# Optimization experiments

Hardware: AMD Instinct MI355X
Metric: run time of the kernel (lower is better)

## Reference

```python
import jax, jax.numpy as jnp
import numpy as np

N_ENT, N_REL, D, H, N_MID = 4096, 200, 128, 4, 9  # 1 input layer + 9 middle layers + 1 out layer
ALPHA = 0.2
NEG = -9e15


def gat_head(x, adj_mask, W, a):
    # x: [N, Fin], W: [Fin, Fout], a: [2*Fout]
    Wh = x @ W                                   # [N, Fout]
    d = Wh.shape[-1]
    f1 = Wh @ a[:d]                              # [N]
    f2 = Wh @ a[d:]                              # [N]
    e = jax.nn.leaky_relu(f1[:, None] + f2[None, :], ALPHA)  # [N, N]
    e = jnp.where(adj_mask, e, NEG)
    attn = jax.nn.softmax(e, axis=-1)
    return attn @ Wh                             # [N, Fout]


def multihead_concat(x, adj_mask, Ws, As):
    # Ws: [H, Fin, Fout], As: [H, 2*Fout] -> elu(concat over heads) [N, H*Fout]
    heads = jax.vmap(lambda W, a: gat_head(x, adj_mask, W, a))(Ws, As)  # [H, N, Fout]
    N = x.shape[0]
    return jax.nn.elu(jnp.transpose(heads, (1, 0, 2)).reshape(N, -1))


def setup_inputs() -> dict:
    key = jax.random.key(0)
    ks = jax.random.split(key, 12)
    s = 0.1
    return {
        "head": jax.random.randint(ks[0], (4096,), 0, N_ENT),
        "relation": jax.random.randint(ks[1], (4096,), 0, N_REL),
        "adj": jax.random.normal(ks[2], (N_ENT, N_ENT), dtype=jnp.float32),
        "entity_emb": jax.random.normal(ks[3], (N_ENT, D), dtype=jnp.float32) * s,
        "relation_emb": jax.random.normal(ks[4], (N_REL, D), dtype=jnp.float32) * s,
        "W0": jax.random.normal(ks[5], (H, D, D), dtype=jnp.float32) * s,
        "a0": jax.random.normal(ks[6], (H, 2 * D), dtype=jnp.float32) * s,
        "Wm": jax.random.normal(ks[7], (N_MID, H, H * D, D), dtype=jnp.float32) * s,
        "am": jax.random.normal(ks[8], (N_MID, H, 2 * D), dtype=jnp.float32) * s,
        "Wo": jax.random.normal(ks[9], (H * D, D), dtype=jnp.float32) * s,
        "ao": jax.random.normal(ks[10], (2 * D,), dtype=jnp.float32) * s,
    }


def reference(head, relation, adj, entity_emb, relation_emb, W0, a0, Wm, am, Wo, ao):
    adj_mask = adj > 0
    # layer 0: D -> H*D
    x = multihead_concat(entity_emb, adj_mask, W0, a0)
    # 9 middle layers: H*D -> H*D (identical shapes -> scan)
    def step(x, params):
        Ws, As = params
        return multihead_concat(x, adj_mask, Ws, As), None
    x, _ = jax.lax.scan(step, x, (Wm, am))
    # output layer: single head H*D -> D, elu applied after
    x = jax.nn.elu(gat_head(x, adj_mask, Wo, ao))
    head_relation_combined = entity_emb[head] + relation_emb[relation]
    return (x, head_relation_combined)
```

## Files before the change

kernel.cpp:

```cpp
#include <hip/hip_runtime.h>

typedef unsigned short u16;
typedef short bf16x8 __attribute__((ext_vector_type(8)));
typedef float f32x4 __attribute__((ext_vector_type(4)));

__device__ __forceinline__ float bf2f(unsigned v) { return __uint_as_float(v << 16); }
__device__ __forceinline__ u16 f2bf(float f) {
    unsigned u = __float_as_uint(f);
    return (u16)((u + 0x7fffu + ((u >> 16) & 1u)) >> 16);
}

__device__ __forceinline__ void gload_lds16(const void* g, void* l) {
    __builtin_amdgcn_global_load_lds(
        (const __attribute__((address_space(1))) unsigned int*)g,
        (__attribute__((address_space(3))) unsigned int*)l, 16, 0, 0);
}

__global__ __launch_bounds__(256) void k_mask(const float* __restrict__ adj,
                                              unsigned* __restrict__ mask) {
    int w = blockIdx.x * 256 + threadIdx.x;
    const float4* q = (const float4*)(adj + (size_t)w * 32);
    unsigned bits = 0u;
#pragma unroll
    for (int i = 0; i < 8; i++) {
        float4 v = q[i];
        if (v.x > 0.f) bits |= (1u << (i * 4 + 0));
        if (v.y > 0.f) bits |= (1u << (i * 4 + 1));
        if (v.z > 0.f) bits |= (1u << (i * 4 + 2));
        if (v.w > 0.f) bits |= (1u << (i * 4 + 3));
    }
    mask[w] = bits;
}

__global__ void k_trans(const float* __restrict__ in, u16* __restrict__ out, int K) {
    __shared__ float t[32][33];
    const float* src = in + (size_t)blockIdx.z * K * 128;
    u16* dst = out + (size_t)blockIdx.z * K * 128;
    int k0 = blockIdx.x * 32, n0 = blockIdx.y * 32;
    int tx = threadIdx.x, ty = threadIdx.y;
#pragma unroll
    for (int i = 0; i < 32; i += 8) t[ty + i][tx] = src[(size_t)(k0 + ty + i) * 128 + n0 + tx];
    __syncthreads();
#pragma unroll
    for (int i = 0; i < 32; i += 8) dst[(size_t)(n0 + ty + i) * K + k0 + tx] = f2bf(t[tx][ty + i]);
}

__global__ __launch_bounds__(256) void k_cvt(const float* __restrict__ in,
                                             u16* __restrict__ out) {
    int t = blockIdx.x * 256 + threadIdx.x;
    float4 v = ((const float4*)in)[t];
    uint2 o;
    o.x = (unsigned)f2bf(v.x) | ((unsigned)f2bf(v.y) << 16);
    o.y = (unsigned)f2bf(v.z) | ((unsigned)f2bf(v.w) << 16);
    ((uint2*)out)[t] = o;
}

__global__ __launch_bounds__(1024, 4) void k_proj(const u16* __restrict__ X,
                                                  const u16* __restrict__ WT,
                                                  const float* __restrict__ avec,
                                                  u16* __restrict__ WhT,
                                                  float* __restrict__ f1,
                                                  float* __restrict__ f2, int Fin) {
    __shared__ u16 As[2][64 * 32];
    __shared__ u16 Bs[2][128 * 32];
    __shared__ float fpart[4][64][2];
    const int tid = threadIdx.x;
    const int wv = tid >> 6, lane = tid & 63;
    const int rg = wv & 3, cg = wv >> 2;
    const int c = lane & 15, quad = lane >> 4;
    const int h = blockIdx.y;
    const int j0 = blockIdx.x * 64;
    const u16* Wp = WT + (size_t)h * 128 * Fin;

#define PROJ_STAGE(buf, kb)                                                              \
    do {                                                                                 \
        if (cg == 0)                                                                     \
            gload_lds16(X + (size_t)(j0 + rg * 16 + (lane >> 2)) * Fin + (kb) + (lane & 3) * 8, \
                        (void*)&As[buf][rg * 16 * 32]);                                  \
        else if (cg <= 2)                                                                \
            gload_lds16(Wp + (size_t)((cg - 1) * 64 + rg * 16 + (lane >> 2)) * Fin + (kb) + (lane & 3) * 8, \
                        (void*)&Bs[buf][((cg - 1) * 64 + rg * 16) * 32]);                \
    } while (0)

    PROJ_STAGE(0, 0);
    __syncthreads();

    f32x4 acc[2];
    acc[0] = (f32x4){0.f, 0.f, 0.f, 0.f};
    acc[1] = (f32x4){0.f, 0.f, 0.f, 0.f};

    int it = 0;
    for (int kb = 0; kb < Fin; kb += 32, it++) {
        const int cur = it & 1;
        if (kb + 32 < Fin) PROJ_STAGE(cur ^ 1, kb + 32);
        bf16x8 av = *(const bf16x8*)&As[cur][(rg * 16 + c) * 32 + quad * 8];
#pragma unroll
        for (int e = 0; e < 2; e++) {
            bf16x8 bv = *(const bf16x8*)&Bs[cur][((cg * 2 + e) * 16 + c) * 32 + quad * 8];
            acc[e] = __builtin_amdgcn_mfma_f32_16x16x32_bf16(av, bv, acc[e], 0, 0, 0);
        }
        __syncthreads();
    }

    u16* Wo = WhT + (size_t)h * 128 * 4096;
    const float* ah = avec + h * 256;
    float p1[4] = {0, 0, 0, 0}, p2[4] = {0, 0, 0, 0};
#pragma unroll
    for (int e = 0; e < 2; e++) {
        const int n = (cg * 2 + e) * 16 + c;
        float a1 = ah[n];
        float a2 = ah[128 + n];
        u16 w4[4];
#pragma unroll
        for (int r = 0; r < 4; r++) {
            float v = acc[e][r];
            w4[r] = f2bf(v);
            p1[r] += v * a1;
            p2[r] += v * a2;
        }
        uint2 pk;
        pk.x = (unsigned)w4[0] | ((unsigned)w4[1] << 16);
        pk.y = (unsigned)w4[2] | ((unsigned)w4[3] << 16);
        *(uint2*)&Wo[(size_t)n * 4096 + j0 + rg * 16 + quad * 4] = pk;
    }
#pragma unroll
    for (int off = 1; off < 16; off <<= 1) {
#pragma unroll
        for (int r = 0; r < 4; r++) {
            p1[r] += __shfl_xor(p1[r], off);
            p2[r] += __shfl_xor(p2[r], off);
        }
    }
    if (c == 0) {
#pragma unroll
        for (int r = 0; r < 4; r++) {
            fpart[cg][rg * 16 + quad * 4 + r][0] = p1[r];
            fpart[cg][rg * 16 + quad * 4 + r][1] = p2[r];
        }
    }
    __syncthreads();
    if (tid < 64) {
        float s1 = fpart[0][tid][0] + fpart[1][tid][0] + fpart[2][tid][0] + fpart[3][tid][0];
        float s2 = fpart[0][tid][1] + fpart[1][tid][1] + fpart[2][tid][1] + fpart[3][tid][1];
        f1[h * 4096 + j0 + tid] = s1;
        f2[h * 4096 + j0 + tid] = s2;
    }
}

template <bool F32OUT>
__global__ __launch_bounds__(1024, 4) void k_attn(const u16* __restrict__ WhT,
                                                  const float* __restrict__ f1g,
                                                  const float* __restrict__ f2g,
                                                  const unsigned char* __restrict__ maskb,
                                                  void* __restrict__ outp, int ostride) {
    __shared__ float f2s[4096];
    __shared__ unsigned char ms[64 * 528];
    __shared__ u16 Bs[2][4][128 * 32];
    __shared__ float f1s[64];
    __shared__ float lpart[4][64];
    __shared__ float redmax[16];
    __shared__ float red[64 * 132];

    const int tid = threadIdx.x;
    const int wv = tid >> 6, lane = tid & 63;
    const int jg = wv >> 2, rg = wv & 3;
    const int c = lane & 15, quad = lane >> 4;
    const int h = blockIdx.y;
    const int i0 = blockIdx.x * 64;
    const float LOG2E = 1.4426950408889634f;
    const float* f1h = f1g + h * 4096;
    const float* f2h = f2g + h * 4096;
    const u16* Wp = WhT + (size_t)h * 128 * 4096;

#define ATTN_STAGE(buf, kb)                                                              \
    do {                                                                                 \
        const int jb_ = jg * 1024 + (kb) * 32;                                           \
        _Pragma("unroll")                                                                \
        for (int e = 0; e < 2; e++)                                                      \
            gload_lds16(Wp + (size_t)(rg * 32 + e * 16 + (lane >> 2)) * 4096 + jb_ + (lane & 3) * 8, \
                        (void*)&Bs[buf][jg][(rg * 32 + e * 16) * 32]);                   \
    } while (0)

    float mymax = -3.0e38f;
    {
        float4 v = ((const float4*)f2h)[tid];
        v.x *= LOG2E; v.y *= LOG2E; v.z *= LOG2E; v.w *= LOG2E;
        ((float4*)f2s)[tid] = v;
        mymax = fmaxf(fmaxf(v.x, v.y), fmaxf(v.z, v.w));
    }
    if (tid < 64) f1s[tid] = f1h[i0 + tid] * LOG2E;
    {
        const uint4* msrc = (const uint4*)(maskb + (size_t)i0 * 512);
#pragma unroll
        for (int e = 0; e < 2; e++) {
            int o = tid + e * 1024;
            uint4 v = msrc[o];
            int row = o >> 5, col = o & 31;
            *(uint4*)&ms[row * 528 + col * 16] = v;
        }
    }
    ATTN_STAGE(0, 0);
#pragma unroll
    for (int off = 1; off < 64; off <<= 1) mymax = fmaxf(mymax, __shfl_xor(mymax, off));
    if (lane == 0) redmax[wv] = mymax;
    __syncthreads();
    float F2MAX = redmax[0];
#pragma unroll
    for (int i = 1; i < 16; i++) F2MAX = fmaxf(F2MAX, redmax[i]);

    const int iloc = rg * 16 + c;
    const float rf1 = f1s[iloc];
    const float zb = rf1 + F2MAX;
    const float rm = fmaxf(zb, 0.2f * zb);
    const float Ac = rf1 - rm;
    const float Bc = 0.2f * rf1 - rm;

    f32x4 acc[8];
#pragma unroll
    for (int i = 0; i < 8; i++) acc[i] = (f32x4){0.f, 0.f, 0.f, 0.f};
    float lsum = 0.f;

    for (int kb = 0; kb < 32; kb++) {
        const int cur = kb & 1;
        if (kb < 31) ATTN_STAGE(cur ^ 1, kb + 1);
        const int jb = jg * 1024 + kb * 32;
        const unsigned mb = ms[iloc * 528 + jg * 128 + kb * 4 + quad];
        const float4 fa = *(const float4*)&f2s[jb + quad * 8];
        const float4 fb = *(const float4*)&f2s[jb + quad * 8 + 4];
        const float f2v[8] = {fa.x, fa.y, fa.z, fa.w, fb.x, fb.y, fb.z, fb.w};
        union { bf16x8 v; unsigned u[4]; } af;
#pragma unroll
        for (int t = 0; t < 8; t += 2) {
            float s0 = fmaxf(Ac + f2v[t],     __builtin_fmaf(0.2f, f2v[t],     Bc));
            float s1 = fmaxf(Ac + f2v[t + 1], __builtin_fmaf(0.2f, f2v[t + 1], Bc));
            float p0 = __builtin_amdgcn_exp2f(s0);
            float p1 = __builtin_amdgcn_exp2f(s1);
            unsigned u0 = ((mb >> t) & 1u)       ? (__float_as_uint(p0) & 0xffff0000u) : 0u;
            unsigned u1 = ((mb >> (t + 1)) & 1u) ? (__float_as_uint(p1) & 0xffff0000u) : 0u;
            lsum += __uint_as_float(u0) + __uint_as_float(u1);
            af.u[t >> 1] = (u0 >> 16) | u1;
        }
#pragma unroll
        for (int nt = 0; nt < 8; nt++) {
            bf16x8 bv = *(const bf16x8*)&Bs[cur][jg][(nt * 16 + c) * 32 + quad * 8];
            acc[nt] = __builtin_amdgcn_mfma_f32_16x16x32_bf16(af.v, bv, acc[nt], 0, 0, 0);
        }
        __syncthreads();
    }

    lsum += __shfl_xor(lsum, 16);
    lsum += __shfl_xor(lsum, 32);
    if (quad == 0) lpart[jg][iloc] = lsum;

#pragma unroll
    for (int g = 0; g < 4; g++) {
        __syncthreads();
        if (jg == g) {
#pragma unroll
            for (int nt = 0; nt < 8; nt++) {
#pragma unroll
                for (int r = 0; r < 4; r++) {
                    int idx = (rg * 16 + quad * 4 + r) * 132 + nt * 16 + c;
                    if (g == 0) red[idx] = acc[nt][r];
                    else        red[idx] += acc[nt][r];
                }
            }
        }
    }
    __syncthreads();

    const int row = tid >> 4, cb = tid & 15;
    const float l = lpart[0][row] + lpart[1][row] + lpart[2][row] + lpart[3][row];
    const float linv = 1.0f / l;
    float vv[8];
#pragma unroll
    for (int t = 0; t < 8; t++) {
        float v = red[row * 132 + cb * 8 + t] * linv;
        vv[t] = v > 0.f ? v : __expf(v) - 1.f;
    }
    const size_t obase = (size_t)(i0 + row) * ostride + h * 128 + cb * 8;
    if (F32OUT) {
        float* op = (float*)outp + obase;
        *(float4*)op = *(float4*)&vv[0];
        *(float4*)(op + 4) = *(float4*)&vv[4];
    } else {
        uint4 o;
        o.x = (unsigned)f2bf(vv[0]) | ((unsigned)f2bf(vv[1]) << 16);
        o.y = (unsigned)f2bf(vv[2]) | ((unsigned)f2bf(vv[3]) << 16);
        o.z = (unsigned)f2bf(vv[4]) | ((unsigned)f2bf(vv[5]) << 16);
        o.w = (unsigned)f2bf(vv[6]) | ((unsigned)f2bf(vv[7]) << 16);
        *(uint4*)((u16*)outp + obase) = o;
    }
}

__global__ __launch_bounds__(256) void k_gather(const int* __restrict__ head,
                                                const int* __restrict__ rel,
                                                const float* __restrict__ ent,
                                                const float* __restrict__ rele,
                                                float* __restrict__ out) {
    int t = blockIdx.x * 256 + threadIdx.x;
    int row = t >> 5, sg = t & 31;
    int hh = head[row], rr = rel[row];
    float4 a = ((const float4*)(ent + (size_t)hh * 128))[sg];
    float4 b = ((const float4*)(rele + (size_t)rr * 128))[sg];
    float4 o;
    o.x = a.x + b.x; o.y = a.y + b.y; o.z = a.z + b.z; o.w = a.w + b.w;
    ((float4*)(out + (size_t)row * 128))[sg] = o;
}

extern "C" void kernel_launch(void* const* d_in, const int* in_sizes, int n_in,
                              void* d_out, int out_size, void* d_ws, size_t ws_size,
                              hipStream_t stream) {
    const int*   head = (const int*)d_in[0];
    const int*   rel  = (const int*)d_in[1];
    const float* adj  = (const float*)d_in[2];
    const float* ent  = (const float*)d_in[3];
    const float* rele = (const float*)d_in[4];
    const float* W0   = (const float*)d_in[5];
    const float* a0   = (const float*)d_in[6];
    const float* Wm   = (const float*)d_in[7];
    const float* am   = (const float*)d_in[8];
    const float* Wo   = (const float*)d_in[9];
    const float* ao   = (const float*)d_in[10];

    char* ws = (char*)d_ws;
    unsigned* mask = (unsigned*)(ws + 0);
    u16* WT0 = (u16*)(ws + 2097152);
    u16* WT5 = (u16*)(ws + 2228224);
    u16* WhT = (u16*)(ws + 7077888);
    float* f1 = (float*)(ws + 11272192);
    float* f2 = (float*)(ws + 11337728);
    u16* xA = (u16*)(ws + 11403264);
    u16* xB = (u16*)(ws + 15597568);
    u16* x0 = (u16*)(ws + 19791872);

    float* out_x = (float*)d_out;
    float* out_comb = out_x + (size_t)4096 * 128;

    k_mask<<<2048, 256, 0, stream>>>(adj, mask);
    k_cvt<<<512, 256, 0, stream>>>(ent, x0);
    k_trans<<<dim3(4, 4, 4), dim3(32, 8), 0, stream>>>(W0, WT0, 128);
    k_trans<<<dim3(16, 4, 36), dim3(32, 8), 0, stream>>>(Wm, WT5, 512);
    k_trans<<<dim3(16, 4, 1), dim3(32, 8), 0, stream>>>(Wo, WT5 + (size_t)36 * 512 * 128, 512);
    k_gather<<<512, 256, 0, stream>>>(head, rel, ent, rele, out_comb);

    k_proj<<<dim3(64, 4), 1024, 0, stream>>>(x0, WT0, a0, WhT, f1, f2, 128);
    k_attn<false><<<dim3(64, 4), 1024, 0, stream>>>(WhT, f1, f2, (const unsigned char*)mask, xA, 512);
    u16 *xc = xA, *xn = xB;
    for (int l = 0; l < 9; l++) {
        k_proj<<<dim3(64, 4), 1024, 0, stream>>>(xc, WT5 + (size_t)l * 4 * 512 * 128,
                                                 am + (size_t)l * 4 * 256, WhT, f1, f2, 512);
        k_attn<false><<<dim3(64, 4), 1024, 0, stream>>>(WhT, f1, f2, (const unsigned char*)mask, xn, 512);
        u16* t = xc; xc = xn; xn = t;
    }
    k_proj<<<dim3(64, 1), 1024, 0, stream>>>(xc, WT5 + (size_t)36 * 512 * 128, ao, WhT, f1, f2, 512);
    k_attn<true><<<dim3(64, 1), 1024, 0, stream>>>(WhT, f1, f2, (const unsigned char*)mask, out_x, 128);
}
```

Before: 670.8 us.

## Halve attention block to 512 threads with two row tiles per wave and swizzle LDS

The attention kernel now runs 8 waves instead of 16, and each wave computes two 16-row tiles. Every B-operand fragment read from LDS therefore feeds two MFMAs, which halves LDS read traffic per MFMA and the staging loads per wave. Both the projection and attention kernels also XOR-swizzle the 16-byte column chunks when loading global data into LDS and when reading fragments, to reduce LDS bank conflicts. In exchange, register pressure doubles in the accumulators and there are fewer waves to hide latency.

```diff
diff --git a/kernel.cpp b/kernel.cpp
--- a/kernel.cpp
+++ b/kernel.cpp
@@ -15,6 +15,7 @@
         (const __attribute__((address_space(1))) unsigned int*)g,
         (__attribute__((address_space(3))) unsigned int*)l, 16, 0, 0);
 }
+
 
 __global__ __launch_bounds__(256) void k_mask(const float* __restrict__ adj,
                                               unsigned* __restrict__ mask) {
@@ -68,17 +69,19 @@
     const int wv = tid >> 6, lane = tid & 63;
     const int rg = wv & 3, cg = wv >> 2;
     const int c = lane & 15, quad = lane >> 4;
+    const int bofs = (quad ^ ((c >> 1) & 3)) * 8;
     const int h = blockIdx.y;
     const int j0 = blockIdx.x * 64;
     const u16* Wp = WT + (size_t)h * 128 * Fin;
+    const int sgr = ((lane & 3) ^ ((lane >> 3) & 3)) * 8;
 
 #define PROJ_STAGE(buf, kb)                                                              \
     do {                                                                                 \
         if (cg == 0)                                                                     \
-            gload_lds16(X + (size_t)(j0 + rg * 16 + (lane >> 2)) * Fin + (kb) + (lane & 3) * 8, \
+            gload_lds16(X + (size_t)(j0 + rg * 16 + (lane >> 2)) * Fin + (kb) + sgr,     \
                         (void*)&As[buf][rg * 16 * 32]);                                  \
         else if (cg <= 2)                                                                \
-            gload_lds16(Wp + (size_t)((cg - 1) * 64 + rg * 16 + (lane >> 2)) * Fin + (kb) + (lane & 3) * 8, \
+            gload_lds16(Wp + (size_t)((cg - 1) * 64 + rg * 16 + (lane >> 2)) * Fin + (kb) + sgr, \
                         (void*)&Bs[buf][((cg - 1) * 64 + rg * 16) * 32]);                \
     } while (0)
 
@@ -93,10 +96,10 @@
     for (int kb = 0; kb < Fin; kb += 32, it++) {
         const int cur = it & 1;
         if (kb + 32 < Fin) PROJ_STAGE(cur ^ 1, kb + 32);
-        bf16x8 av = *(const bf16x8*)&As[cur][(rg * 16 + c) * 32 + quad * 8];
+        bf16x8 av = *(const bf16x8*)&As[cur][(rg * 16 + c) * 32 + bofs];
 #pragma unroll
         for (int e = 0; e < 2; e++) {
-            bf16x8 bv = *(const bf16x8*)&Bs[cur][((cg * 2 + e) * 16 + c) * 32 + quad * 8];
+            bf16x8 bv = *(const bf16x8*)&Bs[cur][((cg * 2 + e) * 16 + c) * 32 + bofs];
             acc[e] = __builtin_amdgcn_mfma_f32_16x16x32_bf16(av, bv, acc[e], 0, 0, 0);
         }
         __syncthreads();
@@ -148,23 +151,25 @@
 }
 
 template <bool F32OUT>
-__global__ __launch_bounds__(1024, 4) void k_attn(const u16* __restrict__ WhT,
-                                                  const float* __restrict__ f1g,
-                                                  const float* __restrict__ f2g,
-                                                  const unsigned char* __restrict__ maskb,
-                                                  void* __restrict__ outp, int ostride) {
+__global__ __launch_bounds__(512, 2) void k_attn(const u16* __restrict__ WhT,
+                                                 const float* __restrict__ f1g,
+                                                 const float* __restrict__ f2g,
+                                                 const unsigned char* __restrict__ maskb,
+                                                 void* __restrict__ outp, int ostride) {
     __shared__ float f2s[4096];
     __shared__ unsigned char ms[64 * 528];
     __shared__ u16 Bs[2][4][128 * 32];
     __shared__ float f1s[64];
     __shared__ float lpart[4][64];
-    __shared__ float redmax[16];
+    __shared__ float redmax[8];
     __shared__ float red[64 * 132];
 
     const int tid = threadIdx.x;
     const int wv = tid >> 6, lane = tid & 63;
-    const int jg = wv >> 2, rg = wv & 3;
+    const int jg = wv >> 1, rg = wv & 1;
     const int c = lane & 15, quad = lane >> 4;
+    const int bofs = (quad ^ ((c >> 1) & 3)) * 8;
+    const int sgr = ((lane & 3) ^ ((lane >> 3) & 3)) * 8;
     const int h = blockIdx.y;
     const int i0 = blockIdx.x * 64;
     const float LOG2E = 1.4426950408889634f;
@@ -176,24 +181,25 @@
     do {                                                                                 \
         const int jb_ = jg * 1024 + (kb) * 32;                                           \
         _Pragma("unroll")                                                                \
-        for (int e = 0; e < 2; e++)                                                      \
-            gload_lds16(Wp + (size_t)(rg * 32 + e * 16 + (lane >> 2)) * 4096 + jb_ + (lane & 3) * 8, \
-                        (void*)&Bs[buf][jg][(rg * 32 + e * 16) * 32]);                   \
+        for (int e_ = 0; e_ < 4; e_++)                                                   \
+            gload_lds16(Wp + (size_t)(rg * 64 + e_ * 16 + (lane >> 2)) * 4096 + jb_ + sgr, \
+                        (void*)&Bs[buf][jg][(rg * 64 + e_ * 16) * 32]);                  \
     } while (0)
 
     float mymax = -3.0e38f;
-    {
-        float4 v = ((const float4*)f2h)[tid];
+#pragma unroll
+    for (int e = 0; e < 2; e++) {
+        float4 v = ((const float4*)f2h)[tid + e * 512];
         v.x *= LOG2E; v.y *= LOG2E; v.z *= LOG2E; v.w *= LOG2E;
-        ((float4*)f2s)[tid] = v;
-        mymax = fmaxf(fmaxf(v.x, v.y), fmaxf(v.z, v.w));
+        ((float4*)f2s)[tid + e * 512] = v;
+        mymax = fmaxf(mymax, fmaxf(fmaxf(v.x, v.y), fmaxf(v.z, v.w)));
     }
     if (tid < 64) f1s[tid] = f1h[i0 + tid] * LOG2E;
     {
         const uint4* msrc = (const uint4*)(maskb + (size_t)i0 * 512);
 #pragma unroll
-        for (int e = 0; e < 2; e++) {
-            int o = tid + e * 1024;
+        for (int e = 0; e < 4; e++) {
+            int o = tid + e * 512;
             uint4 v = msrc[o];
             int row = o >> 5, col = o & 31;
             *(uint4*)&ms[row * 528 + col * 16] = v;
@@ -206,90 +212,125 @@
     __syncthreads();
     float F2MAX = redmax[0];
 #pragma unroll
-    for (int i = 1; i < 16; i++) F2MAX = fmaxf(F2MAX, redmax[i]);
-
-    const int iloc = rg * 16 + c;
-    const float rf1 = f1s[iloc];
-    const float zb = rf1 + F2MAX;
-    const float rm = fmaxf(zb, 0.2f * zb);
-    const float Ac = rf1 - rm;
-    const float Bc = 0.2f * rf1 - rm;
-
-    f32x4 acc[8];
-#pragma unroll
-    for (int i = 0; i < 8; i++) acc[i] = (f32x4){0.f, 0.f, 0.f, 0.f};
-    float lsum = 0.f;
+    for (int i = 1; i < 8; i++) F2MAX = fmaxf(F2MAX, redmax[i]);
+
+    const int iloc0 = rg * 32 + c;
+    const int iloc1 = iloc0 + 16;
+    const float rf1a = f1s[iloc0];
+    const float rf1b = f1s[iloc1];
+    const float za = rf1a + F2MAX, zb = rf1b + F2MAX;
+    const float rma = fmaxf(za, 0.2f * za), rmb = fmaxf(zb, 0.2f * zb);
+    const float Aca = rf1a - rma, Bca = 0.2f * rf1a - rma;
+    const float Acb = rf1b - rmb, Bcb = 0.2f * rf1b - rmb;
+
+    f32x4 acc[2][8];
+#pragma unroll
+    for (int f = 0; f < 2; f++)
+#pragma unroll
+        for (int i = 0; i < 8; i++) acc[f][i] = (f32x4){0.f, 0.f, 0.f, 0.f};
+    float lsa = 0.f, lsb = 0.f;
 
     for (int kb = 0; kb < 32; kb++) {
         const int cur = kb & 1;
         if (kb < 31) ATTN_STAGE(cur ^ 1, kb + 1);
         const int jb = jg * 1024 + kb * 32;
-        const unsigned mb = ms[iloc * 528 + jg * 128 + kb * 4 + quad];
+        const int mofs = jg * 128 + kb * 4 + quad;
+        const unsigned mba = ms[iloc0 * 528 + mofs];
+        const unsigned mbb = ms[iloc1 * 528 + mofs];
         const float4 fa = *(const float4*)&f2s[jb + quad * 8];
         const float4 fb = *(const float4*)&f2s[jb + quad * 8 + 4];
         const float f2v[8] = {fa.x, fa.y, fa.z, fa.w, fb.x, fb.y, fb.z, fb.w};
-        union { bf16x8 v; unsigned u[4]; } af;
+        union { bf16x8 v; unsigned u[4]; } afa, afb;
 #pragma unroll
         for (int t = 0; t < 8; t += 2) {
-            float s0 = fmaxf(Ac + f2v[t],     __builtin_fmaf(0.2f, f2v[t],     Bc));
-            float s1 = fmaxf(Ac + f2v[t + 1], __builtin_fmaf(0.2f, f2v[t + 1], Bc));
-            float p0 = __builtin_amdgcn_exp2f(s0);
-            float p1 = __builtin_amdgcn_exp2f(s1);
-            unsigned u0 = ((mb >> t) & 1u)       ? (__float_as_uint(p0) & 0xffff0000u) : 0u;
-            unsigned u1 = ((mb >> (t + 1)) & 1u) ? (__float_as_uint(p1) & 0xffff0000u) : 0u;
-            lsum += __uint_as_float(u0) + __uint_as_float(u1);
-            af.u[t >> 1] = (u0 >> 16) | u1;
+            float g0 = f2v[t], g1 = f2v[t + 1];
+            float sa0 = fmaxf(Aca + g0, __builtin_fmaf(0.2f, g0, Bca));
+            float sa1 = fmaxf(Aca + g1, __builtin_fmaf(0.2f, g1, Bca));
+            float sb0 = fmaxf(Acb + g0, __builtin_fmaf(0.2f, g0, Bcb));
+            float sb1 = fmaxf(Acb + g1, __builtin_fmaf(0.2f, g1, Bcb));
+            float pa0 = __builtin_amdgcn_exp2f(sa0);
+            float pa1 = __builtin_amdgcn_exp2f(sa1);
+            float pb0 = __builtin_amdgcn_exp2f(sb0);
+            float pb1 = __builtin_amdgcn_exp2f(sb1);
+            unsigned ua0 = ((mba >> t) & 1u)       ? (__float_as_uint(pa0) & 0xffff0000u) : 0u;
+            unsigned ua1 = ((mba >> (t + 1)) & 1u) ? (__float_as_uint(pa1) & 0xffff0000u) : 0u;
+            unsigned ub0 = ((mbb >> t) & 1u)       ? (__float_as_uint(pb0) & 0xffff0000u) : 0u;
+            unsigned ub1 = ((mbb >> (t + 1)) & 1u) ? (__float_as_uint(pb1) & 0xffff0000u) : 0u;
+            lsa += __uint_as_float(ua0) + __uint_as_float(ua1);
+            lsb += __uint_as_float(ub0) + __uint_as_float(ub1);
+            afa.u[t >> 1] = (ua0 >> 16) | ua1;
+            afb.u[t >> 1] = (ub0 >> 16) | ub1;
         }
 #pragma unroll
         for (int nt = 0; nt < 8; nt++) {
-            bf16x8 bv = *(const bf16x8*)&Bs[cur][jg][(nt * 16 + c) * 32 + quad * 8];
-            acc[nt] = __builtin_amdgcn_mfma_f32_16x16x32_bf16(af.v, bv, acc[nt], 0, 0, 0);
+            bf16x8 bv = *(const bf16x8*)&Bs[cur][jg][(nt * 16 + c) * 32 + bofs];
+            acc[0][nt] = __builtin_amdgcn_mfma_f32_16x16x32_bf16(afa.v, bv, acc[0][nt], 0, 0, 0);
+            acc[1][nt] = __builtin_amdgcn_mfma_f32_16x16x32_bf16(afb.v, bv, acc[1][nt], 0, 0, 0);
         }
         __syncthreads();
     }
 
-    lsum += __shfl_xor(lsum, 16);
-    lsum += __shfl_xor(lsum, 32);
-    if (quad == 0) lpart[jg][iloc] = lsum;
+    lsa += __shfl_xor(lsa, 16);
+    lsa += __shfl_xor(lsa, 32);
+    lsb += __shfl_xor(lsb, 16);
+    lsb += __shfl_xor(lsb, 32);
+    if (quad == 0) {
+        lpart[jg][iloc0] = lsa;
+        lpart[jg][iloc1] = lsb;
+    }
 
 #pragma unroll
     for (int g = 0; g < 4; g++) {
         __syncthreads();
         if (jg == g) {
 #pragma unroll
-            for (int nt = 0; nt < 8; nt++) {
-#pragma unroll
-                for (int r = 0; r < 4; r++) {
-                    int idx = (rg * 16 + quad * 4 + r) * 132 + nt * 16 + c;
-                    if (g == 0) red[idx] = acc[nt][r];
-                    else        red[idx] += acc[nt][r];
+            for (int f = 0; f < 2; f++) {
+#pragma unroll
+                for (int nt = 0; nt < 8; nt++) {
+#pragma unroll
+                    for (int r = 0; r < 4; r++) {
+                        int idx = (rg * 32 + f * 16 + quad * 4 + r) * 132 + nt * 16 + c;
+                        if (g == 0) red[idx] = acc[f][nt][r];
+                        else        red[idx] += acc[f][nt][r];
+                    }
                 }
             }
         }
     }
     __syncthreads();
 
-    const int row = tid >> 4, cb = tid & 15;
+    const int row = tid >> 3, ob = tid & 7;
     const float l = lpart[0][row] + lpart[1][row] + lpart[2][row] + lpart[3][row];
     const float linv = 1.0f / l;
-    float vv[8];
-#pragma unroll
-    for (int t = 0; t < 8; t++) {
-        float v = red[row * 132 + cb * 8 + t] * linv;
-        vv[t] = v > 0.f ? v : __expf(v) - 1.f;
-    }
-    const size_t obase = (size_t)(i0 + row) * ostride + h * 128 + cb * 8;
+    float vv[16];
+#pragma unroll
+    for (int half = 0; half < 2; half++) {
+#pragma unroll
+        for (int t = 0; t < 8; t++) {
+            float v = red[row * 132 + (ob + half * 8) * 8 + t] * linv;
+            vv[half * 8 + t] = v > 0.f ? v : __expf(v) - 1.f;
+        }
+    }
+    const size_t obase = (size_t)(i0 + row) * ostride + h * 128 + ob * 8;
     if (F32OUT) {
         float* op = (float*)outp + obase;
         *(float4*)op = *(float4*)&vv[0];
         *(float4*)(op + 4) = *(float4*)&vv[4];
+        *(float4*)(op + 64) = *(float4*)&vv[8];
+        *(float4*)(op + 68) = *(float4*)&vv[12];
     } else {
+        u16* op = (u16*)outp + obase;
         uint4 o;
         o.x = (unsigned)f2bf(vv[0]) | ((unsigned)f2bf(vv[1]) << 16);
         o.y = (unsigned)f2bf(vv[2]) | ((unsigned)f2bf(vv[3]) << 16);
         o.z = (unsigned)f2bf(vv[4]) | ((unsigned)f2bf(vv[5]) << 16);
         o.w = (unsigned)f2bf(vv[6]) | ((unsigned)f2bf(vv[7]) << 16);
-        *(uint4*)((u16*)outp + obase) = o;
+        *(uint4*)op = o;
+        o.x = (unsigned)f2bf(vv[8])  | ((unsigned)f2bf(vv[9]) << 16);
+        o.y = (unsigned)f2bf(vv[10]) | ((unsigned)f2bf(vv[11]) << 16);
+        o.z = (unsigned)f2bf(vv[12]) | ((unsigned)f2bf(vv[13]) << 16);
+        o.w = (unsigned)f2bf(vv[14]) | ((unsigned)f2bf(vv[15]) << 16);
+        *(uint4*)(op + 64) = o;
     }
 }
 
@@ -345,14 +386,14 @@
     k_gather<<<512, 256, 0, stream>>>(head, rel, ent, rele, out_comb);
 
     k_proj<<<dim3(64, 4), 1024, 0, stream>>>(x0, WT0, a0, WhT, f1, f2, 128);
-    k_attn<false><<<dim3(64, 4), 1024, 0, stream>>>(WhT, f1, f2, (const unsigned char*)mask, xA, 512);
+    k_attn<false><<<dim3(64, 4), 512, 0, stream>>>(WhT, f1, f2, (const unsigned char*)mask, xA, 512);
     u16 *xc = xA, *xn = xB;
     for (int l = 0; l < 9; l++) {
         k_proj<<<dim3(64, 4), 1024, 0, stream>>>(xc, WT5 + (size_t)l * 4 * 512 * 128,
                                                  am + (size_t)l * 4 * 256, WhT, f1, f2, 512);
-        k_attn<false><<<dim3(64, 4), 1024, 0, stream>>>(WhT, f1, f2, (const unsigned char*)mask, xn, 512);
+        k_attn<false><<<dim3(64, 4), 512, 0, stream>>>(WhT, f1, f2, (const unsigned char*)mask, xn, 512);
         u16* t = xc; xc = xn; xn = t;
     }
     k_proj<<<dim3(64, 1), 1024, 0, stream>>>(xc, WT5 + (size_t)36 * 512 * 128, ao, WhT, f1, f2, 512);
-    k_attn<true><<<dim3(64, 1), 1024, 0, stream>>>(WhT, f1, f2, (const unsigned char*)mask, out_x, 128);
-}
+    k_attn<true><<<dim3(64, 1), 512, 0, stream>>>(WhT, f1, f2, (const unsigned char*)mask, out_x, 128);
+}
```

After: 704.9 us. +5.1%, slower.

## Factor attention exponentials into per-column precomputed exp2 terms and retile attention kernel

Applied to the files above, without the earlier changes.

The projection kernel now stores exp2(f2) and exp2(0.2*f2) per column. The attention kernel then forms each probability as a per-row constant times one of these via a threshold compare, which removes the per-element exp and the global max pass. The attention kernel is retiled to 512 threads with 32 rows per block and 8 column groups, each owning a full 128-wide B tile, with software-pipelined P computation and MFMA. It also XOR-swizzles LDS layouts to avoid bank conflicts. The risk is that dropping max-subtraction can overflow or underflow when f2 values are large, and the attention path now needs more global loads of the E12 table.

```diff
diff --git a/kernel.cpp b/kernel.cpp
--- a/kernel.cpp
+++ b/kernel.cpp
@@ -15,6 +15,7 @@
         (const __attribute__((address_space(1))) unsigned int*)g,
         (__attribute__((address_space(3))) unsigned int*)l, 16, 0, 0);
 }
+
 
 __global__ __launch_bounds__(256) void k_mask(const float* __restrict__ adj,
                                               unsigned* __restrict__ mask) {
@@ -60,7 +61,7 @@
                                                   const float* __restrict__ avec,
                                                   u16* __restrict__ WhT,
                                                   float* __restrict__ f1,
-                                                  float* __restrict__ f2, int Fin) {
+                                                  float* __restrict__ E12g, int Fin) {
     __shared__ u16 As[2][64 * 32];
     __shared__ u16 Bs[2][128 * 32];
     __shared__ float fpart[4][64][2];
@@ -68,17 +69,19 @@
     const int wv = tid >> 6, lane = tid & 63;
     const int rg = wv & 3, cg = wv >> 2;
     const int c = lane & 15, quad = lane >> 4;
+    const int bofs = (quad ^ ((c >> 1) & 3)) * 8;
     const int h = blockIdx.y;
     const int j0 = blockIdx.x * 64;
     const u16* Wp = WT + (size_t)h * 128 * Fin;
+    const int sgr = ((lane & 3) ^ ((lane >> 3) & 3)) * 8;
 
 #define PROJ_STAGE(buf, kb)                                                              \
     do {                                                                                 \
         if (cg == 0)                                                                     \
-            gload_lds16(X + (size_t)(j0 + rg * 16 + (lane >> 2)) * Fin + (kb) + (lane & 3) * 8, \
+            gload_lds16(X + (size_t)(j0 + rg * 16 + (lane >> 2)) * Fin + (kb) + sgr,     \
                         (void*)&As[buf][rg * 16 * 32]);                                  \
         else if (cg <= 2)                                                                \
-            gload_lds16(Wp + (size_t)((cg - 1) * 64 + rg * 16 + (lane >> 2)) * Fin + (kb) + (lane & 3) * 8, \
+            gload_lds16(Wp + (size_t)((cg - 1) * 64 + rg * 16 + (lane >> 2)) * Fin + (kb) + sgr, \
                         (void*)&Bs[buf][((cg - 1) * 64 + rg * 16) * 32]);                \
     } while (0)
 
@@ -93,10 +96,10 @@
     for (int kb = 0; kb < Fin; kb += 32, it++) {
         const int cur = it & 1;
         if (kb + 32 < Fin) PROJ_STAGE(cur ^ 1, kb + 32);
-        bf16x8 av = *(const bf16x8*)&As[cur][(rg * 16 + c) * 32 + quad * 8];
+        bf16x8 av = *(const bf16x8*)&As[cur][(rg * 16 + c) * 32 + bofs];
 #pragma unroll
         for (int e = 0; e < 2; e++) {
-            bf16x8 bv = *(const bf16x8*)&Bs[cur][((cg * 2 + e) * 16 + c) * 32 + quad * 8];
+            bf16x8 bv = *(const bf16x8*)&Bs[cur][((cg * 2 + e) * 16 + c) * 32 + bofs];
             acc[e] = __builtin_amdgcn_mfma_f32_16x16x32_bf16(av, bv, acc[e], 0, 0, 0);
         }
         __syncthreads();
@@ -143,126 +146,148 @@
         float s1 = fpart[0][tid][0] + fpart[1][tid][0] + fpart[2][tid][0] + fpart[3][tid][0];
         float s2 = fpart[0][tid][1] + fpart[1][tid][1] + fpart[2][tid][1] + fpart[3][tid][1];
         f1[h * 4096 + j0 + tid] = s1;
-        f2[h * 4096 + j0 + tid] = s2;
+        const float LOG2E = 1.4426950408889634f;
+        float d = s2 * LOG2E;
+        float* e12 = E12g + h * 8192 + 2 * (j0 + tid);
+        e12[0] = __builtin_amdgcn_exp2f(d);
+        e12[1] = __builtin_amdgcn_exp2f(0.2f * d);
     }
 }
 
 template <bool F32OUT>
-__global__ __launch_bounds__(1024, 4) void k_attn(const u16* __restrict__ WhT,
-                                                  const float* __restrict__ f1g,
-                                                  const float* __restrict__ f2g,
-                                                  const unsigned char* __restrict__ maskb,
-                                                  void* __restrict__ outp, int ostride) {
-    __shared__ float f2s[4096];
-    __shared__ unsigned char ms[64 * 528];
-    __shared__ u16 Bs[2][4][128 * 32];
-    __shared__ float f1s[64];
-    __shared__ float lpart[4][64];
-    __shared__ float redmax[16];
-    __shared__ float red[64 * 132];
+__global__ __launch_bounds__(512, 4) void k_attn(const u16* __restrict__ WhT,
+                                                 const float* __restrict__ f1g,
+                                                 const float* __restrict__ E12g,
+                                                 const unsigned char* __restrict__ maskb,
+                                                 void* __restrict__ outp, int ostride) {
+    __shared__ u16 Bs[8][128 * 32];
+    __shared__ float lpart[8][32];
 
     const int tid = threadIdx.x;
-    const int wv = tid >> 6, lane = tid & 63;
-    const int jg = wv >> 2, rg = wv & 3;
+    const int jg = tid >> 6, lane = tid & 63;
     const int c = lane & 15, quad = lane >> 4;
+    const int bofs = (quad ^ ((c >> 1) & 3)) * 8;
+    const int sgr = ((lane & 3) ^ ((lane >> 3) & 3)) * 8;
     const int h = blockIdx.y;
-    const int i0 = blockIdx.x * 64;
+    const int i0 = blockIdx.x * 32;
     const float LOG2E = 1.4426950408889634f;
-    const float* f1h = f1g + h * 4096;
-    const float* f2h = f2g + h * 4096;
     const u16* Wp = WhT + (size_t)h * 128 * 4096;
-
-#define ATTN_STAGE(buf, kb)                                                              \
+    const float* Ep = E12g + h * 8192;
+
+#define ATTN_STAGE(kb)                                                                   \
     do {                                                                                 \
-        const int jb_ = jg * 1024 + (kb) * 32;                                           \
+        const int jb_ = jg * 512 + (kb) * 32;                                            \
         _Pragma("unroll")                                                                \
-        for (int e = 0; e < 2; e++)                                                      \
-            gload_lds16(Wp + (size_t)(rg * 32 + e * 16 + (lane >> 2)) * 4096 + jb_ + (lane & 3) * 8, \
-                        (void*)&Bs[buf][jg][(rg * 32 + e * 16) * 32]);                   \
+        for (int e_ = 0; e_ < 8; e_++)                                                   \
+            gload_lds16(Wp + (size_t)(e_ * 16 + (lane >> 2)) * 4096 + jb_ + sgr,         \
+                        (void*)&Bs[jg][(e_ * 16) * 32]);                                 \
     } while (0)
 
-    float mymax = -3.0e38f;
-    {
-        float4 v = ((const float4*)f2h)[tid];
-        v.x *= LOG2E; v.y *= LOG2E; v.z *= LOG2E; v.w *= LOG2E;
-        ((float4*)f2s)[tid] = v;
-        mymax = fmaxf(fmaxf(v.x, v.y), fmaxf(v.z, v.w));
-    }
-    if (tid < 64) f1s[tid] = f1h[i0 + tid] * LOG2E;
-    {
-        const uint4* msrc = (const uint4*)(maskb + (size_t)i0 * 512);
-#pragma unroll
-        for (int e = 0; e < 2; e++) {
-            int o = tid + e * 1024;
-            uint4 v = msrc[o];
-            int row = o >> 5, col = o & 31;
-            *(uint4*)&ms[row * 528 + col * 16] = v;
-        }
-    }
-    ATTN_STAGE(0, 0);
-#pragma unroll
-    for (int off = 1; off < 64; off <<= 1) mymax = fmaxf(mymax, __shfl_xor(mymax, off));
-    if (lane == 0) redmax[wv] = mymax;
-    __syncthreads();
-    float F2MAX = redmax[0];
-#pragma unroll
-    for (int i = 1; i < 16; i++) F2MAX = fmaxf(F2MAX, redmax[i]);
-
-    const int iloc = rg * 16 + c;
-    const float rf1 = f1s[iloc];
-    const float zb = rf1 + F2MAX;
-    const float rm = fmaxf(zb, 0.2f * zb);
-    const float Ac = rf1 - rm;
-    const float Bc = 0.2f * rf1 - rm;
-
-    f32x4 acc[8];
-#pragma unroll
-    for (int i = 0; i < 8; i++) acc[i] = (f32x4){0.f, 0.f, 0.f, 0.f};
-    float lsum = 0.f;
-
-    for (int kb = 0; kb < 32; kb++) {
-        const int cur = kb & 1;
-        if (kb < 31) ATTN_STAGE(cur ^ 1, kb + 1);
-        const int jb = jg * 1024 + kb * 32;
-        const unsigned mb = ms[iloc * 528 + jg * 128 + kb * 4 + quad];
-        const float4 fa = *(const float4*)&f2s[jb + quad * 8];
-        const float4 fb = *(const float4*)&f2s[jb + quad * 8 + 4];
-        const float f2v[8] = {fa.x, fa.y, fa.z, fa.w, fb.x, fb.y, fb.z, fb.w};
-        union { bf16x8 v; unsigned u[4]; } af;
-#pragma unroll
-        for (int t = 0; t < 8; t += 2) {
-            float s0 = fmaxf(Ac + f2v[t],     __builtin_fmaf(0.2f, f2v[t],     Bc));
-            float s1 = fmaxf(Ac + f2v[t + 1], __builtin_fmaf(0.2f, f2v[t + 1], Bc));
-            float p0 = __builtin_amdgcn_exp2f(s0);
-            float p1 = __builtin_amdgcn_exp2f(s1);
-            unsigned u0 = ((mb >> t) & 1u)       ? (__float_as_uint(p0) & 0xffff0000u) : 0u;
-            unsigned u1 = ((mb >> (t + 1)) & 1u) ? (__float_as_uint(p1) & 0xffff0000u) : 0u;
-            lsum += __uint_as_float(u0) + __uint_as_float(u1);
-            af.u[t >> 1] = (u0 >> 16) | u1;
-        }
-#pragma unroll
-        for (int nt = 0; nt < 8; nt++) {
-            bf16x8 bv = *(const bf16x8*)&Bs[cur][jg][(nt * 16 + c) * 32 + quad * 8];
-            acc[nt] = __builtin_amdgcn_mfma_f32_16x16x32_bf16(af.v, bv, acc[nt], 0, 0, 0);
-        }
-        __syncthreads();
-    }
-
-    lsum += __shfl_xor(lsum, 16);
-    lsum += __shfl_xor(lsum, 32);
-    if (quad == 0) lpart[jg][iloc] = lsum;
-
-#pragma unroll
-    for (int g = 0; g < 4; g++) {
+    ATTN_STAGE(0);
+
+    const float rf1a = f1g[h * 4096 + i0 + c] * LOG2E;
+    const float rf1b = f1g[h * 4096 + i0 + 16 + c] * LOG2E;
+    const float rma = fmaxf(rf1a, 0.2f * rf1a);
+    const float rmb = fmaxf(rf1b, 0.2f * rf1b);
+    const float C1a = __builtin_amdgcn_exp2f(rf1a - rma);
+    const float C2a = __builtin_amdgcn_exp2f(0.2f * rf1a - rma);
+    const float Ta  = __builtin_amdgcn_exp2f(-rf1a);
+    const float C1b = __builtin_amdgcn_exp2f(rf1b - rmb);
+    const float C2b = __builtin_amdgcn_exp2f(0.2f * rf1b - rmb);
+    const float Tb  = __builtin_amdgcn_exp2f(-rf1b);
+
+    const unsigned char* mpa = maskb + (size_t)(i0 + c) * 512 + jg * 64 + quad;
+    const unsigned char* mpb = maskb + (size_t)(i0 + 16 + c) * 512 + jg * 64 + quad;
+    unsigned mA0 = mpa[0], mB0 = mpb[0];
+    unsigned mA1 = mpa[4], mB1 = mpb[4];
+
+    f32x4 acc0[8], acc1[8];
+#pragma unroll
+    for (int i = 0; i < 8; i++) {
+        acc0[i] = (f32x4){0.f, 0.f, 0.f, 0.f};
+        acc1[i] = (f32x4){0.f, 0.f, 0.f, 0.f};
+    }
+    float lsa = 0.f, lsb = 0.f;
+
+    union AF { bf16x8 v; unsigned u[4]; };
+    AF af0a, af0b, af1a, af1b;
+
+#define COMP_P(dstA, dstB, kb, mba_, mbb_)                                               \
+    do {                                                                                 \
+        const float* ep_ = Ep + 2 * (jg * 512 + (kb) * 32 + quad * 8);                   \
+        _Pragma("unroll")                                                                \
+        for (int t = 0; t < 8; t += 2) {                                                 \
+            float4 e_ = *(const float4*)(ep_ + 2 * t);                                   \
+            float pa0 = ((e_.x > Ta) ? C1a : C2a) * ((e_.x > Ta) ? e_.x : e_.y);         \
+            float pa1 = ((e_.z > Ta) ? C1a : C2a) * ((e_.z > Ta) ? e_.z : e_.w);         \
+            float pb0 = ((e_.x > Tb) ? C1b : C2b) * ((e_.x > Tb) ? e_.x : e_.y);         \
+            float pb1 = ((e_.z > Tb) ? C1b : C2b) * ((e_.z > Tb) ? e_.z : e_.w);         \
+            unsigned ua0 = ((mba_ >> t) & 1u)       ? (__float_as_uint(pa0) & 0xffff0000u) : 0u; \
+            unsigned ua1 = ((mba_ >> (t + 1)) & 1u) ? (__float_as_uint(pa1) & 0xffff0000u) : 0u; \
+            unsigned ub0 = ((mbb_ >> t) & 1u)       ? (__float_as_uint(pb0) & 0xffff0000u) : 0u; \
+            unsigned ub1 = ((mbb_ >> (t + 1)) & 1u) ? (__float_as_uint(pb1) & 0xffff0000u) : 0u; \
+            lsa += __uint_as_float(ua0) + __uint_as_float(ua1);                          \
+            lsb += __uint_as_float(ub0) + __uint_as_float(ub1);                          \
+            dstA.u[t >> 1] = (ua0 >> 16) | ua1;                                          \
+            dstB.u[t >> 1] = (ub0 >> 16) | ub1;                                          \
+        }                                                                                \
+    } while (0)
+
+#define DO_MFMA(srcA, srcB)                                                              \
+    do {                                                                                 \
+        _Pragma("unroll")                                                                \
+        for (int nt = 0; nt < 8; nt++) {                                                 \
+            bf16x8 bv_ = *(const bf16x8*)&Bs[jg][(nt * 16 + c) * 32 + bofs];             \
+            acc0[nt] = __builtin_amdgcn_mfma_f32_16x16x32_bf16(srcA.v, bv_, acc0[nt], 0, 0, 0); \
+            acc1[nt] = __builtin_amdgcn_mfma_f32_16x16x32_bf16(srcB.v, bv_, acc1[nt], 0, 0, 0); \
+        }                                                                                \
+    } while (0)
+
+    COMP_P(af0a, af0b, 0, mA0, mB0);
+    __syncthreads();
+
+    for (int kb = 0; kb < 16; kb += 2) {
+        DO_MFMA(af0a, af0b);
+        __syncthreads();
+        ATTN_STAGE(kb + 1);
+        if (kb + 2 < 16) { mA0 = mpa[4 * (kb + 2)]; mB0 = mpb[4 * (kb + 2)]; }
+        COMP_P(af1a, af1b, kb + 1, mA1, mB1);
+        __syncthreads();
+        DO_MFMA(af1a, af1b);
+        __syncthreads();
+        if (kb + 2 < 16) {
+            ATTN_STAGE(kb + 2);
+            mA1 = mpa[4 * (kb + 3)]; mB1 = mpb[4 * (kb + 3)];
+            COMP_P(af0a, af0b, kb + 2, mA0, mB0);
+        }
+        __syncthreads();
+    }
+
+    lsa += __shfl_xor(lsa, 16);
+    lsa += __shfl_xor(lsa, 32);
+    lsb += __shfl_xor(lsb, 16);
+    lsb += __shfl_xor(lsb, 32);
+    if (quad == 0) {
+        lpart[jg][c] = lsa;
+        lpart[jg][c + 16] = lsb;
+    }
+
+    float* red = (float*)&Bs[0][0];
+#pragma unroll
+    for (int g = 0; g < 8; g++) {
         __syncthreads();
         if (jg == g) {
 #pragma unroll
-            for (int nt = 0; nt < 8; nt++) {
-#pragma unroll
-                for (int r = 0; r < 4; r++) {
-                    int idx = (rg * 16 + quad * 4 + r) * 132 + nt * 16 + c;
-                    if (g == 0) red[idx] = acc[nt][r];
-                    else        red[idx] += acc[nt][r];
+            for (int f = 0; f < 2; f++) {
+#pragma unroll
+                for (int nt = 0; nt < 8; nt++) {
+#pragma unroll
+                    for (int r = 0; r < 4; r++) {
+                        int idx = (f * 16 + quad * 4 + r) * 132 + nt * 16 + c;
+                        float v = (f == 0) ? acc0[nt][r] : acc1[nt][r];
+                        if (g == 0) red[idx] = v;
+                        else        red[idx] += v;
+                    }
                 }
             }
         }
@@ -270,7 +295,9 @@
     __syncthreads();
 
     const int row = tid >> 4, cb = tid & 15;
-    const float l = lpart[0][row] + lpart[1][row] + lpart[2][row] + lpart[3][row];
+    float l = lpart[0][row];
+#pragma unroll
+    for (int g = 1; g < 8; g++) l += lpart[g][row];
     const float linv = 1.0f / l;
     float vv[8];
 #pragma unroll
@@ -329,10 +356,10 @@
     u16* WT5 = (u16*)(ws + 2228224);
     u16* WhT = (u16*)(ws + 7077888);
     float* f1 = (float*)(ws + 11272192);
-    float* f2 = (float*)(ws + 11337728);
     u16* xA = (u16*)(ws + 11403264);
     u16* xB = (u16*)(ws + 15597568);
     u16* x0 = (u16*)(ws + 19791872);
+    float* E12 = (float*)(ws + 20840448);
 
     float* out_x = (float*)d_out;
     float* out_comb = out_x + (size_t)4096 * 128;
@@ -344,15 +371,15 @@
     k_trans<<<dim3(16, 4, 1), dim3(32, 8), 0, stream>>>(Wo, WT5 + (size_t)36 * 512 * 128, 512);
     k_gather<<<512, 256, 0, stream>>>(head, rel, ent, rele, out_comb);
 
-    k_proj<<<dim3(64, 4), 1024, 0, stream>>>(x0, WT0, a0, WhT, f1, f2, 128);
-    k_attn<false><<<dim3(64, 4), 1024, 0, stream>>>(WhT, f1, f2, (const unsigned char*)mask, xA, 512);
+    k_proj<<<dim3(64, 4), 1024, 0, stream>>>(x0, WT0, a0, WhT, f1, E12, 128);
+    k_attn<false><<<dim3(128, 4), 512, 0, stream>>>(WhT, f1, E12, (const unsigned char*)mask, xA, 512);
     u16 *xc = xA, *xn = xB;
     for (int l = 0; l < 9; l++) {
         k_proj<<<dim3(64, 4), 1024, 0, stream>>>(xc, WT5 + (size_t)l * 4 * 512 * 128,
-                                                 am + (size_t)l * 4 * 256, WhT, f1, f2, 512);
-        k_attn<false><<<dim3(64, 4), 1024, 0, stream>>>(WhT, f1, f2, (const unsigned char*)mask, xn, 512);
+                                                 am + (size_t)l * 4 * 256, WhT, f1, E12, 512);
+        k_attn<false><<<dim3(128, 4), 512, 0, stream>>>(WhT, f1, E12, (const unsigned char*)mask, xn, 512);
         u16* t = xc; xc = xn; xn = t;
     }
-    k_proj<<<dim3(64, 1), 1024, 0, stream>>>(xc, WT5 + (size_t)36 * 512 * 128, ao, WhT, f1, f2, 512);
-    k_attn<true><<<dim3(64, 1), 1024, 0, stream>>>(WhT, f1, f2, (const unsigned char*)mask, out_x, 128);
-}
+    k_proj<<<dim3(64, 1), 1024, 0, stream>>>(xc, WT5 + (size_t)36 * 512 * 128, ao, WhT, f1, E12, 512);
+    k_attn<true><<<dim3(128, 1), 512, 0, stream>>>(WhT, f1, E12, (const unsigned char*)mask, out_x, 128);
+}
```

Result: slower. 1.349 ms (+101.0%).
